# Kernel optimization log

Hardware: AMD Instinct MI355X
Metric: run time of the kernel (lower is better)

## Reference

```python
import jax, jax.numpy as jnp
import numpy as np

LMAX = 3
N_NODES = 8192
N_CHANNELS = 64


def _build_instructions():
    """Build sparse CG instruction lists (mu_1, mu_2, mu_3) sorted by mu_3,
    mirroring the path enumeration in TensorProductCuda.__init__."""
    off = {l: l * l for l in range(LMAX + 1)}  # offset of l-block in sph-harm layout
    mu1, mu2, mu3 = [], [], []
    offset3 = 0
    for l1 in range(LMAX + 1):
        for l2 in range(LMAX + 1):
            for l3 in range(abs(l1 - l2), min(l1 + l2, LMAX) + 1):
                k = min(2 * l1 + 1, 2 * l2 + 1)  # nnz pairs per output m3
                for m3 in range(2 * l3 + 1):
                    for m1 in range(k):
                        m2 = (m1 + m3) % (2 * l2 + 1)
                        mu1.append(off[l1] + m1)
                        mu2.append(off[l2] + m2)
                        mu3.append(offset3 + m3)
                offset3 += 2 * l3 + 1
    return (np.asarray(mu1, np.int32), np.asarray(mu2, np.int32),
            np.asarray(mu3, np.int32), offset3)


def setup_inputs() -> dict:
    key = jax.random.key(0)
    k1, k2, k3 = jax.random.split(key, 3)
    mu1, mu2, mu3, dim_out = _build_instructions()  # nnz = 562, dim_out = 156
    dim_in = (LMAX + 1) ** 2  # 16
    x = jax.random.normal(k1, (N_NODES, dim_in, N_CHANNELS), dtype=jnp.float32)
    y = jax.random.normal(k2, (N_NODES, dim_in), dtype=jnp.float32)
    cg = jax.random.normal(k3, (mu1.shape[0],), dtype=jnp.float32) * 0.3
    return {
        "x": x,
        "y": y,
        "cg_coeffs": cg,
        "mu_1": jnp.asarray(mu1),
        "mu_2": jnp.asarray(mu2),
        "mu_3": jnp.asarray(mu3),
        "dim_out": int(dim_out),
    }


def reference(x, y, cg_coeffs, mu_1, mu_2, mu_3, dim_out):
    # gather x components and y sph-harm components per instruction,
    # scale by CG coefficient, scatter-add into output channel mu_3.
    # x: [N, 16, C], y: [N, 16], prod: [N, nnz, C]
    prod = x[:, mu_1, :] * y[:, mu_2][:, :, None] * cg_coeffs[None, :, None]
    out = jnp.zeros((x.shape[0], dim_out, x.shape[2]), dtype=x.dtype)
    out = out.at[:, mu_3, :].add(prod)  # mu_3 is sorted, duplicate-accumulating scatter
    return out
```

## Files before the change

kernel.cpp:

```cpp
#include <hip/hip_runtime.h>
#include <utility>


#define LMAX 3
constexpr int NNZ     = 562;
constexpr int DIM_OUT = 156;
constexpr int DIM_IN  = 16;
constexpr int NCH     = 64;
constexpr int NNODES  = 8192;

struct Tables {
    int mu1[NNZ];
    int mu2[NNZ];
    int seg_start[DIM_OUT + 1];
};

constexpr Tables make_tables() {
    Tables t{};
    int off[LMAX + 1] = {0, 1, 4, 9};
    int idx = 0;
    int offset3 = 0;
    int counts[DIM_OUT] = {};
    for (int l1 = 0; l1 <= LMAX; ++l1) {
        for (int l2 = 0; l2 <= LMAX; ++l2) {
            int lo = l1 > l2 ? l1 - l2 : l2 - l1;
            int hi = (l1 + l2) < LMAX ? (l1 + l2) : LMAX;
            for (int l3 = lo; l3 <= hi; ++l3) {
                int k = (2 * l1 + 1) < (2 * l2 + 1) ? (2 * l1 + 1) : (2 * l2 + 1);
                for (int m3 = 0; m3 < 2 * l3 + 1; ++m3) {
                    for (int m1 = 0; m1 < k; ++m1) {
                        int m2 = (m1 + m3) % (2 * l2 + 1);
                        t.mu1[idx] = off[l1] + m1;
                        t.mu2[idx] = off[l2] + m2;
                        ++idx;
                    }
                    counts[offset3 + m3] += k;
                }
                offset3 += 2 * l3 + 1;
            }
        }
    }
    int acc = 0;
    for (int o = 0; o < DIM_OUT; ++o) {
        t.seg_start[o] = acc;
        acc += counts[o];
    }
    t.seg_start[DIM_OUT] = acc;
    return t;
}

constexpr Tables TBL = make_tables();

template <int I, int E>
__device__ __forceinline__ float seg_sum(const float (&xr)[DIM_IN],
                                         const float (&yv)[DIM_IN],
                                         const float* __restrict__ cg,
                                         float acc) {
    if constexpr (I >= E) {
        return acc;
    } else {
        constexpr int m1 = TBL.mu1[I];
        constexpr int m2 = TBL.mu2[I];
        acc = fmaf(xr[m1] * yv[m2], cg[I], acc);
        return seg_sum<I + 1, E>(xr, yv, cg, acc);
    }
}

template <int O>
__device__ __forceinline__ void emit_out(const float (&xr)[DIM_IN],
                                         const float (&yv)[DIM_IN],
                                         const float* __restrict__ cg,
                                         float* __restrict__ op) {
    constexpr int B = TBL.seg_start[O];
    constexpr int E = TBL.seg_start[O + 1];
    float acc = seg_sum<B, E>(xr, yv, cg, 0.0f);
    __builtin_nontemporal_store(acc, op + O * NCH);
}

template <int... Os>
__device__ __forceinline__ void emit_all(std::integer_sequence<int, Os...>,
                                         const float (&xr)[DIM_IN],
                                         const float (&yv)[DIM_IN],
                                         const float* __restrict__ cg,
                                         float* __restrict__ op) {
    (emit_out<Os>(xr, yv, cg, op), ...);
}

__global__ __launch_bounds__(256) void tp_kernel(
    const float* __restrict__ x,
    const float* __restrict__ y,
    const float* __restrict__ cg,
    float* __restrict__ out)
{
    const int wave = threadIdx.x >> 6;
    const int lane = threadIdx.x & 63;
    const int node = blockIdx.x * 4 + wave;

    const float* xp = x + (size_t)node * (DIM_IN * NCH) + lane;
    float xr[DIM_IN];
#pragma unroll
    for (int k = 0; k < DIM_IN; ++k) xr[k] = xp[k * NCH];

    float yv[DIM_IN];
    const float4* y4 = (const float4*)(y + (size_t)node * DIM_IN);
#pragma unroll
    for (int j = 0; j < 4; ++j) {
        float4 t = y4[j];
        yv[4 * j + 0] = t.x;
        yv[4 * j + 1] = t.y;
        yv[4 * j + 2] = t.z;
        yv[4 * j + 3] = t.w;
    }

    float* op = out + (size_t)node * (DIM_OUT * NCH) + lane;
    emit_all(std::make_integer_sequence<int, DIM_OUT>{}, xr, yv, cg, op);
}

extern "C" void kernel_launch(void* const* d_in, const int* in_sizes, int n_in,
                              void* d_out, int out_size, void* d_ws, size_t ws_size,
                              hipStream_t stream) {
    const float* x  = (const float*)d_in[0];
    const float* y  = (const float*)d_in[1];
    const float* cg = (const float*)d_in[2];
    float* out = (float*)d_out;

    tp_kernel<<<NNODES / 4, 256, 0, stream>>>(x, y, cg, out);
}
```

Measured before the change: 358.3 us.

## Process two channels per lane with float2 and two nodes per wave

Result: no change. 364.5 us (+1.7%).

```diff
diff --git a/kernel.cpp b/kernel.cpp
--- a/kernel.cpp
+++ b/kernel.cpp
@@ -52,34 +52,37 @@
 constexpr Tables TBL = make_tables();
 
 template <int I, int E>
-__device__ __forceinline__ float seg_sum(const float (&xr)[DIM_IN],
-                                         const float (&yv)[DIM_IN],
-                                         const float* __restrict__ cg,
-                                         float acc) {
+__device__ __forceinline__ float2 seg_sum2(const float2 (&xr)[DIM_IN],
+                                           const float (&yv)[DIM_IN],
+                                           const float* __restrict__ cg,
+                                           float2 acc) {
     if constexpr (I >= E) {
         return acc;
     } else {
         constexpr int m1 = TBL.mu1[I];
         constexpr int m2 = TBL.mu2[I];
-        acc = fmaf(xr[m1] * yv[m2], cg[I], acc);
-        return seg_sum<I + 1, E>(xr, yv, cg, acc);
+        const float w = yv[m2];
+        const float c = cg[I];
+        acc.x = fmaf(xr[m1].x * w, c, acc.x);
+        acc.y = fmaf(xr[m1].y * w, c, acc.y);
+        return seg_sum2<I + 1, E>(xr, yv, cg, acc);
     }
 }
 
 template <int O>
-__device__ __forceinline__ void emit_out(const float (&xr)[DIM_IN],
+__device__ __forceinline__ void emit_out(const float2 (&xr)[DIM_IN],
                                          const float (&yv)[DIM_IN],
                                          const float* __restrict__ cg,
                                          float* __restrict__ op) {
     constexpr int B = TBL.seg_start[O];
     constexpr int E = TBL.seg_start[O + 1];
-    float acc = seg_sum<B, E>(xr, yv, cg, 0.0f);
-    __builtin_nontemporal_store(acc, op + O * NCH);
+    float2 acc = seg_sum2<B, E>(xr, yv, cg, make_float2(0.0f, 0.0f));
+    *reinterpret_cast<float2*>(op + O * NCH) = acc;
 }
 
 template <int... Os>
 __device__ __forceinline__ void emit_all(std::integer_sequence<int, Os...>,
-                                         const float (&xr)[DIM_IN],
+                                         const float2 (&xr)[DIM_IN],
                                          const float (&yv)[DIM_IN],
                                          const float* __restrict__ cg,
                                          float* __restrict__ op) {
@@ -94,12 +97,15 @@
 {
     const int wave = threadIdx.x >> 6;
     const int lane = threadIdx.x & 63;
-    const int node = blockIdx.x * 4 + wave;
+    const int sub  = lane >> 5;
+    const int g    = lane & 31;
+    const int node = (blockIdx.x * 4 + wave) * 2 + sub;
 
-    const float* xp = x + (size_t)node * (DIM_IN * NCH) + lane;
-    float xr[DIM_IN];
+    const float* xp = x + (size_t)node * (DIM_IN * NCH) + 2 * g;
+    float2 xr[DIM_IN];
 #pragma unroll
-    for (int k = 0; k < DIM_IN; ++k) xr[k] = xp[k * NCH];
+    for (int k = 0; k < DIM_IN; ++k)
+        xr[k] = *reinterpret_cast<const float2*>(xp + k * NCH);
 
     float yv[DIM_IN];
     const float4* y4 = (const float4*)(y + (size_t)node * DIM_IN);
@@ -112,7 +118,7 @@
         yv[4 * j + 3] = t.w;
     }
 
-    float* op = out + (size_t)node * (DIM_OUT * NCH) + lane;
+    float* op = out + (size_t)node * (DIM_OUT * NCH) + 2 * g;
     emit_all(std::make_integer_sequence<int, DIM_OUT>{}, xr, yv, cg, op);
 }
 
@@ -124,5 +130,5 @@
     const float* cg = (const float*)d_in[2];
     float* out = (float*)d_out;
 
-    tp_kernel<<<NNODES / 4, 256, 0, stream>>>(x, y, cg, out);
+    tp_kernel<<<NNODES / 8, 256, 0, stream>>>(x, y, cg, out);
 }
```
